# Optimization experiments

Hardware: AMD Instinct MI355X
Metric: run time of the kernel (lower is better)

Reference implementation:

```python
import jax, jax.numpy as jnp
import numpy as np

MIN_DEPTH = 0.1
MAX_DEPTH = 100.0
EPS = 1e-10


def setup_inputs() -> dict:
    key = jax.random.key(0)
    k1, k2, k3 = jax.random.split(key, 3)
    B, R, S = 4, 16384, 128
    colors = jax.random.uniform(k1, (B, R, S, 3), dtype=jnp.float32)
    density_logits = jax.random.normal(k2, (B, R, S, 1), dtype=jnp.float32)
    # depths must be monotonically increasing along the sample axis
    depths = jnp.sort(jax.random.uniform(k3, (B, R, S, 1), dtype=jnp.float32) * 50.0, axis=2)
    return {"colors": colors, "density_logits": density_logits, "depths": depths}


def reference(colors, density_logits, depths):
    # midpoints along the sample axis (dim 2)
    colors_mid = (colors[:, :, :-1] + colors[:, :, 1:]) * 0.5          # [B,R,S-1,3]
    dl_mid = (density_logits[:, :, :-1] + density_logits[:, :, 1:]) * 0.5
    depths_mid = (depths[:, :, :-1] + depths[:, :, 1:]) * 0.5          # [B,R,S-1,1]
    deltas = depths[:, :, 1:] - depths[:, :, :-1]

    # density_activation == 'softplus'
    densities_mid = jax.nn.softplus(dl_mid - 1.0)

    alpha = 1.0 - jnp.exp(-densities_mid * deltas)                     # [B,R,S-1,1]
    alpha_shifted = jnp.concatenate(
        [jnp.ones_like(alpha[:, :, :1]), 1.0 - alpha + EPS], axis=-2)
    transmittance = jnp.cumprod(alpha_shifted, axis=-2)[:, :, :-1]
    weights = (alpha + EPS) * transmittance                            # [B,R,S-1,1]
    weight_total = weights.sum(axis=2)                                 # [B,R,1]

    # c_sky is None branch
    weights_all = weights
    composite_rgb = jnp.sum(weights * colors_mid, axis=-2)             # [B,R,3]
    composite_depth = jnp.sum(weights * depths_mid, axis=-2) / (EPS + weight_total)

    composite_depth = jnp.nan_to_num(composite_depth, nan=MAX_DEPTH)
    composite_depth = jnp.clip(composite_depth, MIN_DEPTH, MAX_DEPTH)
    composite_rgb = composite_rgb * 2.0 - 1.0
    return (composite_rgb, composite_depth, weights, weights_all, alpha, depths_mid)
```

## Files before the change

kernel.cpp:

```cpp
#include <hip/hip_runtime.h>
#include <math.h>

namespace {
constexpr int Bn = 4, Rn = 16384, Sn = 128;
constexpr int NRAY = Bn * Rn;
constexpr int SI   = Sn - 1;
constexpr size_t OFF_RGB   = 0;
constexpr size_t OFF_DEPTH = OFF_RGB   + (size_t)NRAY * 3;
constexpr size_t OFF_W     = OFF_DEPTH + (size_t)NRAY;
constexpr size_t OFF_WALL  = OFF_W     + (size_t)NRAY * SI;
constexpr size_t OFF_ALPHA = OFF_WALL  + (size_t)NRAY * SI;
constexpr size_t OFF_DMID  = OFF_ALPHA + (size_t)NRAY * SI;
constexpr float  EPSF      = 1e-10f;
}

template<int CTRL, int ROW_MASK, bool BC>
__device__ __forceinline__ float dpp_mov(float oldv, float src) {
    return __int_as_float(__builtin_amdgcn_update_dpp(
        __float_as_int(oldv), __float_as_int(src), CTRL, ROW_MASK, 0xF, BC));
}

__device__ __forceinline__ float wave_prefix_prod(float s) {
    s *= dpp_mov<0x111, 0xF, false>(1.0f, s);
    s *= dpp_mov<0x112, 0xF, false>(1.0f, s);
    s *= dpp_mov<0x114, 0xF, false>(1.0f, s);
    s *= dpp_mov<0x118, 0xF, false>(1.0f, s);
    s *= dpp_mov<0x142, 0xa, false>(1.0f, s);
    s *= dpp_mov<0x143, 0xc, false>(1.0f, s);
    return s;
}

__device__ __forceinline__ float wave_sum_last(float x) {
    x += dpp_mov<0x111, 0xF, true>(0.0f, x);
    x += dpp_mov<0x112, 0xF, true>(0.0f, x);
    x += dpp_mov<0x114, 0xF, true>(0.0f, x);
    x += dpp_mov<0x118, 0xF, true>(0.0f, x);
    x += dpp_mov<0x142, 0xa, true>(0.0f, x);
    x += dpp_mov<0x143, 0xc, true>(0.0f, x);
    return x;
}

__global__ __launch_bounds__(256) void raymarch_kernel(
    const float* __restrict__ colors,
    const float* __restrict__ dlog,
    const float* __restrict__ depths,
    float* __restrict__ out)
{
    const int gtid = blockIdx.x * 256 + threadIdx.x;
    const int ray  = gtid >> 6;
    const int lane = threadIdx.x & 63;

    const float2* dp = reinterpret_cast<const float2*>(depths) + (size_t)ray * (Sn / 2);
    const float2* gp = reinterpret_cast<const float2*>(dlog)   + (size_t)ray * (Sn / 2);
    const float2* cp = reinterpret_cast<const float2*>(colors) + (size_t)ray * (Sn * 3 / 2);

    float2 d  = dp[lane];
    float2 g  = gp[lane];
    float2 c0 = cp[lane * 3 + 0];
    float2 c1 = cp[lane * 3 + 1];
    float2 c2 = cp[lane * 3 + 2];

    float d2  = dpp_mov<0x130, 0xF, false>(d.x,  d.x);
    float g2  = dpp_mov<0x130, 0xF, false>(g.x,  g.x);
    float cnx = dpp_mov<0x130, 0xF, false>(c0.x, c0.x);
    float cny = dpp_mov<0x130, 0xF, false>(c0.y, c0.y);
    float cnz = dpp_mov<0x130, 0xF, false>(c1.x, c1.x);

    const bool valid1 = (lane < 63);

    float delta0 = d.y - d.x;
    float dm0    = 0.5f * (d.x + d.y);
    float x0     = 0.5f * (g.x + g.y) - 1.0f;
    float cm0x   = 0.5f * (c0.x + c1.y);
    float cm0y   = 0.5f * (c0.y + c2.x);
    float cm0z   = 0.5f * (c1.x + c2.y);

    float delta1 = valid1 ? (d2 - d.y)            : 0.0f;
    float dm1    = valid1 ? 0.5f * (d.y + d2)     : 0.0f;
    float x1     = valid1 ? (0.5f * (g.y + g2) - 1.0f) : 0.0f;
    float cm1x   = valid1 ? 0.5f * (c1.y + cnx)   : 0.0f;
    float cm1y   = valid1 ? 0.5f * (c2.x + cny)   : 0.0f;
    float cm1z   = valid1 ? 0.5f * (c2.y + cnz)   : 0.0f;

    float l0 = __log2f(1.0f + __expf(x0));
    float l1 = __log2f(1.0f + __expf(x1));
    l0 = fminf(l0, 1e30f);
    l1 = fminf(l1, 1e30f);
    float E0 = exp2f(-delta0 * l0);
    float E1 = exp2f(-delta1 * l1);
    float alpha0 = 1.0f - E0;
    float alpha1 = 1.0f - E1;
    float t0 = E0 + EPSF;
    float t1 = valid1 ? (E1 + EPSF) : 1.0f;

    float s  = wave_prefix_prod(t0 * t1);
    float T0 = dpp_mov<0x138, 0xF, false>(1.0f, s);
    float T1 = T0 * t0;

    float w0 = (alpha0 + EPSF) * T0;
    float w1 = valid1 ? (alpha1 + EPSF) * T1 : 0.0f;

    size_t base = (size_t)ray * SI + 2 * lane;
    out[OFF_W     + base] = w0;
    out[OFF_WALL  + base] = w0;
    out[OFF_ALPHA + base] = alpha0;
    out[OFF_DMID  + base] = dm0;
    if (valid1) {
        out[OFF_W     + base + 1] = w1;
        out[OFF_WALL  + base + 1] = w1;
        out[OFF_ALPHA + base + 1] = alpha1;
        out[OFF_DMID  + base + 1] = dm1;
    }

    float wsum = wave_sum_last(w0 + w1);
    float rx   = wave_sum_last(w0 * cm0x + w1 * cm1x);
    float ry   = wave_sum_last(w0 * cm0y + w1 * cm1y);
    float rz   = wave_sum_last(w0 * cm0z + w1 * cm1z);
    float dsum = wave_sum_last(w0 * dm0  + w1 * dm1);

    if (lane == 63) {
        float cd = dsum / (EPSF + wsum);
        if (isnan(cd)) cd = 100.0f;
        cd = fminf(fmaxf(cd, 0.1f), 100.0f);
        out[OFF_RGB + (size_t)ray * 3 + 0] = rx * 2.0f - 1.0f;
        out[OFF_RGB + (size_t)ray * 3 + 1] = ry * 2.0f - 1.0f;
        out[OFF_RGB + (size_t)ray * 3 + 2] = rz * 2.0f - 1.0f;
        out[OFF_DEPTH + ray] = cd;
    }
}

extern "C" void kernel_launch(void* const* d_in, const int* in_sizes, int n_in,
                              void* d_out, int out_size, void* d_ws, size_t ws_size,
                              hipStream_t stream) {
    const float* colors = (const float*)d_in[0];
    const float* dlog   = (const float*)d_in[1];
    const float* depths = (const float*)d_in[2];
    float* out = (float*)d_out;

    dim3 grid(NRAY / 4);
    dim3 block(256);
    hipLaunchKernelGGL(raymarch_kernel, grid, block, 0, stream, colors, dlog, depths, out);
}
```

Before: 261.6 us.

## Process four rays per wave with batched loads and float2 stores on even rays

Each wavefront now handles four rays and issues all their global loads up front before computing, which raises memory-level parallelism per wave. On even-indexed rays, where the output base offset is 8-byte aligned (ray*127 is even), it writes the per-sample outputs as float2 pairs instead of scalar stores. The grid shrinks by four, and register use rises because the inputs for four rays are held at once.

```diff
diff --git a/kernel.cpp b/kernel.cpp
--- a/kernel.cpp
+++ b/kernel.cpp
@@ -5,6 +5,7 @@
 constexpr int Bn = 4, Rn = 16384, Sn = 128;
 constexpr int NRAY = Bn * Rn;
 constexpr int SI   = Sn - 1;
+constexpr int RPW  = 4;
 constexpr size_t OFF_RGB   = 0;
 constexpr size_t OFF_DEPTH = OFF_RGB   + (size_t)NRAY * 3;
 constexpr size_t OFF_W     = OFF_DEPTH + (size_t)NRAY;
@@ -46,86 +47,111 @@
     const float* __restrict__ depths,
     float* __restrict__ out)
 {
-    const int gtid = blockIdx.x * 256 + threadIdx.x;
-    const int ray  = gtid >> 6;
+    const int wid  = (blockIdx.x * 256 + threadIdx.x) >> 6;
     const int lane = threadIdx.x & 63;
+    const int ray0 = wid * RPW;
 
-    const float2* dp = reinterpret_cast<const float2*>(depths) + (size_t)ray * (Sn / 2);
-    const float2* gp = reinterpret_cast<const float2*>(dlog)   + (size_t)ray * (Sn / 2);
-    const float2* cp = reinterpret_cast<const float2*>(colors) + (size_t)ray * (Sn * 3 / 2);
-
-    float2 d  = dp[lane];
-    float2 g  = gp[lane];
-    float2 c0 = cp[lane * 3 + 0];
-    float2 c1 = cp[lane * 3 + 1];
-    float2 c2 = cp[lane * 3 + 2];
-
-    float d2  = dpp_mov<0x130, 0xF, false>(d.x,  d.x);
-    float g2  = dpp_mov<0x130, 0xF, false>(g.x,  g.x);
-    float cnx = dpp_mov<0x130, 0xF, false>(c0.x, c0.x);
-    float cny = dpp_mov<0x130, 0xF, false>(c0.y, c0.y);
-    float cnz = dpp_mov<0x130, 0xF, false>(c1.x, c1.x);
+    float2 d[RPW], g[RPW], c0[RPW], c1[RPW], c2[RPW];
+    #pragma unroll
+    for (int r = 0; r < RPW; ++r) {
+        const int ray = ray0 + r;
+        const float2* dp = reinterpret_cast<const float2*>(depths) + (size_t)ray * (Sn / 2);
+        const float2* gp = reinterpret_cast<const float2*>(dlog)   + (size_t)ray * (Sn / 2);
+        const float2* cp = reinterpret_cast<const float2*>(colors) + (size_t)ray * (Sn * 3 / 2);
+        d[r]  = dp[lane];
+        g[r]  = gp[lane];
+        c0[r] = cp[lane * 3 + 0];
+        c1[r] = cp[lane * 3 + 1];
+        c2[r] = cp[lane * 3 + 2];
+    }
 
     const bool valid1 = (lane < 63);
 
-    float delta0 = d.y - d.x;
-    float dm0    = 0.5f * (d.x + d.y);
-    float x0     = 0.5f * (g.x + g.y) - 1.0f;
-    float cm0x   = 0.5f * (c0.x + c1.y);
-    float cm0y   = 0.5f * (c0.y + c2.x);
-    float cm0z   = 0.5f * (c1.x + c2.y);
+    #pragma unroll
+    for (int r = 0; r < RPW; ++r) {
+        const int ray = ray0 + r;
 
-    float delta1 = valid1 ? (d2 - d.y)            : 0.0f;
-    float dm1    = valid1 ? 0.5f * (d.y + d2)     : 0.0f;
-    float x1     = valid1 ? (0.5f * (g.y + g2) - 1.0f) : 0.0f;
-    float cm1x   = valid1 ? 0.5f * (c1.y + cnx)   : 0.0f;
-    float cm1y   = valid1 ? 0.5f * (c2.x + cny)   : 0.0f;
-    float cm1z   = valid1 ? 0.5f * (c2.y + cnz)   : 0.0f;
+        float d2  = dpp_mov<0x130, 0xF, false>(d[r].x,  d[r].x);
+        float g2  = dpp_mov<0x130, 0xF, false>(g[r].x,  g[r].x);
+        float cnx = dpp_mov<0x130, 0xF, false>(c0[r].x, c0[r].x);
+        float cny = dpp_mov<0x130, 0xF, false>(c0[r].y, c0[r].y);
+        float cnz = dpp_mov<0x130, 0xF, false>(c1[r].x, c1[r].x);
 
-    float l0 = __log2f(1.0f + __expf(x0));
-    float l1 = __log2f(1.0f + __expf(x1));
-    l0 = fminf(l0, 1e30f);
-    l1 = fminf(l1, 1e30f);
-    float E0 = exp2f(-delta0 * l0);
-    float E1 = exp2f(-delta1 * l1);
-    float alpha0 = 1.0f - E0;
-    float alpha1 = 1.0f - E1;
-    float t0 = E0 + EPSF;
-    float t1 = valid1 ? (E1 + EPSF) : 1.0f;
+        float delta0 = d[r].y - d[r].x;
+        float dm0    = 0.5f * (d[r].x + d[r].y);
+        float x0     = 0.5f * (g[r].x + g[r].y) - 1.0f;
+        float cm0x   = 0.5f * (c0[r].x + c1[r].y);
+        float cm0y   = 0.5f * (c0[r].y + c2[r].x);
+        float cm0z   = 0.5f * (c1[r].x + c2[r].y);
 
-    float s  = wave_prefix_prod(t0 * t1);
-    float T0 = dpp_mov<0x138, 0xF, false>(1.0f, s);
-    float T1 = T0 * t0;
+        float delta1 = valid1 ? (d2 - d[r].y)         : 0.0f;
+        float dm1    = valid1 ? 0.5f * (d[r].y + d2)  : 0.0f;
+        float x1     = valid1 ? (0.5f * (g[r].y + g2) - 1.0f) : 0.0f;
+        float cm1x   = valid1 ? 0.5f * (c1[r].y + cnx) : 0.0f;
+        float cm1y   = valid1 ? 0.5f * (c2[r].x + cny) : 0.0f;
+        float cm1z   = valid1 ? 0.5f * (c2[r].y + cnz) : 0.0f;
 
-    float w0 = (alpha0 + EPSF) * T0;
-    float w1 = valid1 ? (alpha1 + EPSF) * T1 : 0.0f;
+        float l0 = __log2f(1.0f + __expf(x0));
+        float l1 = __log2f(1.0f + __expf(x1));
+        l0 = fminf(l0, 1e30f);
+        l1 = fminf(l1, 1e30f);
+        float E0 = exp2f(-delta0 * l0);
+        float E1 = exp2f(-delta1 * l1);
+        float alpha0 = 1.0f - E0;
+        float alpha1 = 1.0f - E1;
+        float t0 = E0 + EPSF;
+        float t1 = valid1 ? (E1 + EPSF) : 1.0f;
 
-    size_t base = (size_t)ray * SI + 2 * lane;
-    out[OFF_W     + base] = w0;
-    out[OFF_WALL  + base] = w0;
-    out[OFF_ALPHA + base] = alpha0;
-    out[OFF_DMID  + base] = dm0;
-    if (valid1) {
-        out[OFF_W     + base + 1] = w1;
-        out[OFF_WALL  + base + 1] = w1;
-        out[OFF_ALPHA + base + 1] = alpha1;
-        out[OFF_DMID  + base + 1] = dm1;
-    }
+        float s  = wave_prefix_prod(t0 * t1);
+        float T0 = dpp_mov<0x138, 0xF, false>(1.0f, s);
+        float T1 = T0 * t0;
 
-    float wsum = wave_sum_last(w0 + w1);
-    float rx   = wave_sum_last(w0 * cm0x + w1 * cm1x);
-    float ry   = wave_sum_last(w0 * cm0y + w1 * cm1y);
-    float rz   = wave_sum_last(w0 * cm0z + w1 * cm1z);
-    float dsum = wave_sum_last(w0 * dm0  + w1 * dm1);
+        float w0 = (alpha0 + EPSF) * T0;
+        float w1 = valid1 ? (alpha1 + EPSF) * T1 : 0.0f;
 
-    if (lane == 63) {
-        float cd = dsum / (EPSF + wsum);
-        if (isnan(cd)) cd = 100.0f;
-        cd = fminf(fmaxf(cd, 0.1f), 100.0f);
-        out[OFF_RGB + (size_t)ray * 3 + 0] = rx * 2.0f - 1.0f;
-        out[OFF_RGB + (size_t)ray * 3 + 1] = ry * 2.0f - 1.0f;
-        out[OFF_RGB + (size_t)ray * 3 + 2] = rz * 2.0f - 1.0f;
-        out[OFF_DEPTH + ray] = cd;
+        const size_t base = (size_t)ray * SI + 2 * lane;
+        if constexpr (true) {
+            if ((r & 1) == 0) {
+                if (valid1) {
+                    *reinterpret_cast<float2*>(out + OFF_W     + base) = make_float2(w0, w1);
+                    *reinterpret_cast<float2*>(out + OFF_WALL  + base) = make_float2(w0, w1);
+                    *reinterpret_cast<float2*>(out + OFF_ALPHA + base) = make_float2(alpha0, alpha1);
+                    *reinterpret_cast<float2*>(out + OFF_DMID  + base) = make_float2(dm0, dm1);
+                } else {
+                    out[OFF_W     + base] = w0;
+                    out[OFF_WALL  + base] = w0;
+                    out[OFF_ALPHA + base] = alpha0;
+                    out[OFF_DMID  + base] = dm0;
+                }
+            } else {
+                out[OFF_W     + base] = w0;
+                out[OFF_WALL  + base] = w0;
+                out[OFF_ALPHA + base] = alpha0;
+                out[OFF_DMID  + base] = dm0;
+                if (valid1) {
+                    out[OFF_W     + base + 1] = w1;
+                    out[OFF_WALL  + base + 1] = w1;
+                    out[OFF_ALPHA + base + 1] = alpha1;
+                    out[OFF_DMID  + base + 1] = dm1;
+                }
+            }
+        }
+
+        float wsum = wave_sum_last(w0 + w1);
+        float rx   = wave_sum_last(w0 * cm0x + w1 * cm1x);
+        float ry   = wave_sum_last(w0 * cm0y + w1 * cm1y);
+        float rz   = wave_sum_last(w0 * cm0z + w1 * cm1z);
+        float dsum = wave_sum_last(w0 * dm0  + w1 * dm1);
+
+        if (lane == 63) {
+            float cd = dsum / (EPSF + wsum);
+            if (isnan(cd)) cd = 100.0f;
+            cd = fminf(fmaxf(cd, 0.1f), 100.0f);
+            out[OFF_RGB + (size_t)ray * 3 + 0] = rx * 2.0f - 1.0f;
+            out[OFF_RGB + (size_t)ray * 3 + 1] = ry * 2.0f - 1.0f;
+            out[OFF_RGB + (size_t)ray * 3 + 2] = rz * 2.0f - 1.0f;
+            out[OFF_DEPTH + ray] = cd;
+        }
     }
 }
 
@@ -137,7 +163,7 @@
     const float* depths = (const float*)d_in[2];
     float* out = (float*)d_out;
 
-    dim3 grid(NRAY / 4);
+    dim3 grid(NRAY / (4 * RPW));
     dim3 block(256);
     hipLaunchKernelGGL(raymarch_kernel, grid, block, 0, stream, colors, dlog, depths, out);
 }
```

Result: slower. 266.9 us (+2.0%).

## Process eight rays per wave with double-buffered asm loads and vector stores

Applied to the files above, without the earlier changes.

Each wave now handles eight consecutive rays rather than one, and the grid shrinks to match. Input loads for the next ray are issued via inline-asm global_load_dwordx2 before computing the current ray, with manual s_waitcnt vmcnt pinning. The aim is to keep memory requests in flight and hide load latency in this bandwidth-bound kernel. Even-indexed rays, whose per-ray output base is 8-byte aligned, write their per-sample outputs as float2 stores to cut store instruction count. The hand-picked vmcnt thresholds ignore that stores also count against vmcnt, so a wait may return before the next ray's loads have finished, which risks reading stale registers.

```diff
diff --git a/kernel.cpp b/kernel.cpp
--- a/kernel.cpp
+++ b/kernel.cpp
@@ -5,6 +5,7 @@
 constexpr int Bn = 4, Rn = 16384, Sn = 128;
 constexpr int NRAY = Bn * Rn;
 constexpr int SI   = Sn - 1;
+constexpr int RPW  = 8;
 constexpr size_t OFF_RGB   = 0;
 constexpr size_t OFF_DEPTH = OFF_RGB   + (size_t)NRAY * 3;
 constexpr size_t OFF_W     = OFF_DEPTH + (size_t)NRAY;
@@ -40,33 +41,23 @@
     return x;
 }
 
-__global__ __launch_bounds__(256) void raymarch_kernel(
-    const float* __restrict__ colors,
-    const float* __restrict__ dlog,
-    const float* __restrict__ depths,
+__device__ __forceinline__ float2 gload2(const float2* p) {
+    float2 r;
+    asm volatile("global_load_dwordx2 %0, %1, off" : "=v"(r) : "v"(p));
+    return r;
+}
+
+template<bool EVEN>
+__device__ __forceinline__ void compute_store(
+    int ray, int lane, bool valid1,
+    float2 d, float2 g, float2 c0, float2 c1, float2 c2,
     float* __restrict__ out)
 {
-    const int gtid = blockIdx.x * 256 + threadIdx.x;
-    const int ray  = gtid >> 6;
-    const int lane = threadIdx.x & 63;
-
-    const float2* dp = reinterpret_cast<const float2*>(depths) + (size_t)ray * (Sn / 2);
-    const float2* gp = reinterpret_cast<const float2*>(dlog)   + (size_t)ray * (Sn / 2);
-    const float2* cp = reinterpret_cast<const float2*>(colors) + (size_t)ray * (Sn * 3 / 2);
-
-    float2 d  = dp[lane];
-    float2 g  = gp[lane];
-    float2 c0 = cp[lane * 3 + 0];
-    float2 c1 = cp[lane * 3 + 1];
-    float2 c2 = cp[lane * 3 + 2];
-
     float d2  = dpp_mov<0x130, 0xF, false>(d.x,  d.x);
     float g2  = dpp_mov<0x130, 0xF, false>(g.x,  g.x);
     float cnx = dpp_mov<0x130, 0xF, false>(c0.x, c0.x);
     float cny = dpp_mov<0x130, 0xF, false>(c0.y, c0.y);
     float cnz = dpp_mov<0x130, 0xF, false>(c1.x, c1.x);
-
-    const bool valid1 = (lane < 63);
 
     float delta0 = d.y - d.x;
     float dm0    = 0.5f * (d.x + d.y);
@@ -100,16 +91,30 @@
     float w0 = (alpha0 + EPSF) * T0;
     float w1 = valid1 ? (alpha1 + EPSF) * T1 : 0.0f;
 
-    size_t base = (size_t)ray * SI + 2 * lane;
-    out[OFF_W     + base] = w0;
-    out[OFF_WALL  + base] = w0;
-    out[OFF_ALPHA + base] = alpha0;
-    out[OFF_DMID  + base] = dm0;
-    if (valid1) {
-        out[OFF_W     + base + 1] = w1;
-        out[OFF_WALL  + base + 1] = w1;
-        out[OFF_ALPHA + base + 1] = alpha1;
-        out[OFF_DMID  + base + 1] = dm1;
+    const size_t base = (size_t)ray * SI + 2 * lane;
+    if (EVEN) {
+        if (valid1) {
+            *reinterpret_cast<float2*>(out + OFF_W     + base) = make_float2(w0, w1);
+            *reinterpret_cast<float2*>(out + OFF_WALL  + base) = make_float2(w0, w1);
+            *reinterpret_cast<float2*>(out + OFF_ALPHA + base) = make_float2(alpha0, alpha1);
+            *reinterpret_cast<float2*>(out + OFF_DMID  + base) = make_float2(dm0, dm1);
+        } else {
+            out[OFF_W     + base] = w0;
+            out[OFF_WALL  + base] = w0;
+            out[OFF_ALPHA + base] = alpha0;
+            out[OFF_DMID  + base] = dm0;
+        }
+    } else {
+        out[OFF_W     + base] = w0;
+        out[OFF_WALL  + base] = w0;
+        out[OFF_ALPHA + base] = alpha0;
+        out[OFF_DMID  + base] = dm0;
+        if (valid1) {
+            out[OFF_W     + base + 1] = w1;
+            out[OFF_WALL  + base + 1] = w1;
+            out[OFF_ALPHA + base + 1] = alpha1;
+            out[OFF_DMID  + base + 1] = dm1;
+        }
     }
 
     float wsum = wave_sum_last(w0 + w1);
@@ -129,6 +134,59 @@
     }
 }
 
+__global__ __launch_bounds__(256) void raymarch_kernel(
+    const float* __restrict__ colors,
+    const float* __restrict__ dlog,
+    const float* __restrict__ depths,
+    float* __restrict__ out)
+{
+    const int wid  = (blockIdx.x * 256 + threadIdx.x) >> 6;
+    const int lane = threadIdx.x & 63;
+    const int ray0 = wid * RPW;
+    const bool valid1 = (lane < 63);
+
+    const float2* dp = reinterpret_cast<const float2*>(depths) + (size_t)ray0 * (Sn / 2) + lane;
+    const float2* gp = reinterpret_cast<const float2*>(dlog)   + (size_t)ray0 * (Sn / 2) + lane;
+    const float2* cp = reinterpret_cast<const float2*>(colors) + (size_t)ray0 * (Sn * 3 / 2) + lane * 3;
+
+    float2 bd[2], bg[2], bc0[2], bc1[2], bc2[2];
+
+#define ISSUE(k)                                                              \
+    do {                                                                      \
+        bd [(k) & 1] = gload2(dp + (k) * (Sn / 2));                           \
+        bg [(k) & 1] = gload2(gp + (k) * (Sn / 2));                           \
+        bc0[(k) & 1] = gload2(cp + (k) * (Sn * 3 / 2) + 0);                   \
+        bc1[(k) & 1] = gload2(cp + (k) * (Sn * 3 / 2) + 1);                   \
+        bc2[(k) & 1] = gload2(cp + (k) * (Sn * 3 / 2) + 2);                   \
+    } while (0)
+
+#define WAITPIN(k, N)                                                         \
+    asm volatile("s_waitcnt vmcnt(" #N ")"                                    \
+        : "+v"(bd[(k) & 1]), "+v"(bg[(k) & 1]),                               \
+          "+v"(bc0[(k) & 1]), "+v"(bc1[(k) & 1]), "+v"(bc2[(k) & 1])          \
+        :                                                                     \
+        : "memory")
+
+#define CS(k)                                                                 \
+    compute_store<(((k) & 1) == 0)>(ray0 + (k), lane, valid1,                 \
+        bd[(k) & 1], bg[(k) & 1], bc0[(k) & 1], bc1[(k) & 1], bc2[(k) & 1],   \
+        out)
+
+    ISSUE(0);
+    ISSUE(1); WAITPIN(0, 5);  CS(0);
+    ISSUE(2); WAITPIN(1, 15); CS(1);
+    ISSUE(3); WAITPIN(2, 15); CS(2);
+    ISSUE(4); WAITPIN(3, 15); CS(3);
+    ISSUE(5); WAITPIN(4, 15); CS(4);
+    ISSUE(6); WAITPIN(5, 15); CS(5);
+    ISSUE(7); WAITPIN(6, 15); CS(6);
+              WAITPIN(7, 10); CS(7);
+
+#undef ISSUE
+#undef WAITPIN
+#undef CS
+}
+
 extern "C" void kernel_launch(void* const* d_in, const int* in_sizes, int n_in,
                               void* d_out, int out_size, void* d_ws, size_t ws_size,
                               hipStream_t stream) {
@@ -137,7 +195,7 @@
     const float* depths = (const float*)d_in[2];
     float* out = (float*)d_out;
 
-    dim3 grid(NRAY / 4);
+    dim3 grid(NRAY / (4 * RPW));
     dim3 block(256);
     hipLaunchKernelGGL(raymarch_kernel, grid, block, 0, stream, colors, dlog, depths, out);
 }
```

After: 273.9 us. 1.05x slower.
